# Kernel optimization log

Hardware: AMD Instinct MI355X
Metric: run time of the kernel (lower is better)

The kernel has to match this reference:

```python
import jax, jax.numpy as jnp
import numpy as np
from jax import lax

N = 20000; E = 640000
D_IN = 64; F1 = 256; H = 256
HEADS = 8; HC = 128; DH = HC // HEADS
NA = 8; MS = 64


def setup_inputs() -> dict:
    key = jax.random.key(0)
    ks = jax.random.split(key, 40)
    def w(k, shape, fan):
        return (jax.random.normal(k, shape, jnp.float32) / np.sqrt(fan)).astype(jnp.float32)
    inp = {}
    inp['state'] = jax.random.normal(ks[0], (N, D_IN), jnp.float32)
    inp['message'] = jax.random.normal(ks[1], (N, MS), jnp.float32)
    inp['edge_index'] = jax.random.randint(ks[2], (2, E), 0, N)
    # fc1 / fc2
    inp['W_fc1'] = w(ks[3], (D_IN, F1), D_IN); inp['b_fc1'] = jnp.zeros((F1,), jnp.float32)
    inp['W_fc2'] = w(ks[4], (MS, F1), MS);    inp['b_fc2'] = jnp.zeros((F1,), jnp.float32)
    # GRU: 2 layers, torch layout W_ih [3H, in], W_hh [3H, H]
    inp['Wih0'] = w(ks[5], (3 * H, F1), F1); inp['Whh0'] = w(ks[6], (3 * H, H), H)
    inp['bih0'] = jnp.zeros((3 * H,), jnp.float32); inp['bhh0'] = jnp.zeros((3 * H,), jnp.float32)
    inp['Wih1'] = w(ks[7], (3 * H, H), H); inp['Whh1'] = w(ks[8], (3 * H, H), H)
    inp['bih1'] = jnp.zeros((3 * H,), jnp.float32); inp['bhh1'] = jnp.zeros((3 * H,), jnp.float32)
    # GAT layer 1: in H -> HEADS heads of DH (concat -> HC)
    inp['Wg1'] = w(ks[9], (H, HC), H)
    inp['as1'] = w(ks[10], (HEADS, DH), DH); inp['ad1'] = w(ks[11], (HEADS, DH), DH)
    inp['bg1'] = jnp.zeros((HC,), jnp.float32)
    # GAT layer 2: HC -> HC
    inp['Wg2'] = w(ks[12], (HC, HC), HC)
    inp['as2'] = w(ks[13], (HEADS, DH), DH); inp['ad2'] = w(ks[14], (HEADS, DH), DH)
    inp['bg2'] = jnp.zeros((HC,), jnp.float32)
    # heads
    inp['Wc'] = w(ks[15], (HC, 1), HC); inp['bc'] = jnp.zeros((1,), jnp.float32)
    inp['Wmu'] = w(ks[16], (HC + H, NA), HC + H); inp['bmu'] = jnp.zeros((NA,), jnp.float32)
    inp['Wm'] = w(ks[17], (HC, MS), HC); inp['bm'] = jnp.zeros((MS,), jnp.float32)
    return inp


def gru_layer(x_seq, Wih, Whh, bih, bhh):
    # x_seq: [N, in]; torch GRUCell math, batch size 1 squeezed
    h_dim = Whh.shape[1]
    def step(h, x):
        gi = x @ Wih.T + bih
        gh = h @ Whh.T + bhh
        ir, iz, inn = jnp.split(gi, 3)
        hr, hz, hn = jnp.split(gh, 3)
        r = jax.nn.sigmoid(ir + hr)
        z = jax.nn.sigmoid(iz + hz)
        n = jnp.tanh(inn + r * hn)
        h_new = (1.0 - z) * n + z * h
        return h_new, h_new
    h0 = jnp.zeros((h_dim,), x_seq.dtype)
    _, ys = lax.scan(step, h0, x_seq)
    return ys  # [N, h_dim]


def gat_conv(x, W, a_src, a_dst, b, src, dst):
    # x: [N, in] -> [N, HEADS*DH], edge softmax over incoming edges per dst node
    n = x.shape[0]
    h = (x @ W).reshape(n, HEADS, DH)
    e_src = jnp.einsum('nhd,hd->nh', h, a_src)  # [N, HEADS]
    e_dst = jnp.einsum('nhd,hd->nh', h, a_dst)
    e = jax.nn.leaky_relu(e_src[src] + e_dst[dst], 0.2)  # [E, HEADS]
    emax = jax.ops.segment_max(e, dst, num_segments=n)
    emax = lax.stop_gradient(jnp.where(jnp.isfinite(emax), emax, 0.0))
    p = jnp.exp(e - emax[dst])
    denom = jax.ops.segment_sum(p, dst, num_segments=n)
    alpha = p / (denom[dst] + 1e-16)  # [E, HEADS]
    msgs = h[src] * alpha[:, :, None]  # [E, HEADS, DH]
    out = jax.ops.segment_sum(msgs, dst, num_segments=n)
    return out.reshape(n, HEADS * DH) + b


def reference(state, message, edge_index, W_fc1, b_fc1, W_fc2, b_fc2,
              Wih0, Whh0, bih0, bhh0, Wih1, Whh1, bih1, bhh1,
              Wg1, as1, ad1, bg1, Wg2, as2, ad2, bg2,
              Wc, bc, Wmu, bmu, Wm, bm):
    src, dst = edge_index[0], edge_index[1]
    x = jax.nn.relu(state @ W_fc1 + b_fc1)          # [N, F1]
    m = jax.nn.relu(message @ W_fc2 + b_fc2)        # [N, F1]
    x = x + m
    x = gru_layer(x, Wih0, Whh0, bih0, bhh0)        # [N, H]
    x = gru_layer(x, Wih1, Whh1, bih1, bhh1)
    x = jax.nn.relu(x)
    xg = gat_conv(x, Wg1, as1, ad1, bg1, src, dst)  # [N, HC]
    xg = jax.nn.relu(xg)
    xg = gat_conv(xg, Wg2, as2, ad2, bg2, src, dst)
    comm = jax.nn.sigmoid(xg @ Wc + bc)             # [N, 1]
    mu = jnp.tanh(jnp.concatenate([x, xg], axis=-1) @ Wmu + bmu)  # [N, NA]
    msg_out = jnp.tanh(xg @ Wm + bm)                # [N, MS]
    return comm, msg_out, mu
```

## Files before the change

### kernel.cpp

```cpp
#include <hip/hip_runtime.h>
#include <stdint.h>

#define N_NODES 20000
#define E_EDGES 640000
#define F1 256
#define HDIM 256
#define G3 768
#define HEADS 8
#define HC 128
#define DH 16
#define NA 8
#define MS 64

typedef _Float16 h2 __attribute__((ext_vector_type(2)));

__device__ __forceinline__ float fdot2(uint32_t a, uint32_t b, float c) {
#if __has_builtin(__builtin_amdgcn_fdot2)
  return __builtin_amdgcn_fdot2(__builtin_bit_cast(h2, a), __builtin_bit_cast(h2, b), c, false);
#else
  h2 x = __builtin_bit_cast(h2, a), y = __builtin_bit_cast(h2, b);
  return c + (float)x[0] * (float)y[0] + (float)x[1] * (float)y[1];
#endif
}

__device__ __forceinline__ float fexp2(float x) { return __builtin_amdgcn_exp2f(x); }
__device__ __forceinline__ float frcp(float x)  { return __builtin_amdgcn_rcpf(x); }
__device__ __forceinline__ float sigm(float x)  { return frcp(1.f + fexp2(-1.44269504f * x)); }
__device__ __forceinline__ float tanh_(float x) {
  x = fminf(20.f, fmaxf(-20.f, x));
  float t = fexp2(2.88539008f * x);
  return (t - 1.f) * frcp(t + 1.f);
}
__device__ __forceinline__ float leaky(float x) { return (x > 0.f) ? x : 0.2f * x; }
__device__ __forceinline__ unsigned fenc(float f) {
  unsigned u = __float_as_uint(f);
  return (u & 0x80000000u) ? ~u : (u | 0x80000000u);
}
__device__ __forceinline__ float fdec(unsigned u) {
  return __uint_as_float((u & 0x80000000u) ? (u ^ 0x80000000u) : ~u);
}

#define GF_BIAS 1
#define GF_RELU_OUT 2
#define GF_ACC 4
#define GF_RELU_A 8
#define GF_BT 16

template <int FLAGS>
__global__ __launch_bounds__(256) void gemm_k(const float* __restrict__ A,
                                              const float* __restrict__ B,
                                              const float* __restrict__ bias,
                                              float* __restrict__ C,
                                              int M, int K, int P) {
  __shared__ float As[64][68];
  __shared__ float Bs[64][68];
  int colTiles = P >> 6;
  int bx = blockIdx.x % colTiles;
  int by = blockIdx.x / colTiles;
  int row0 = by * 64, col0 = bx * 64;
  int tid = threadIdx.x;
  int tx = tid & 15, ty = tid >> 4;
  float acc[4][4] = {};
  for (int k0 = 0; k0 < K; k0 += 64) {
    {
      int r = tid >> 2, kq = (tid & 3) * 16;
      int gr = row0 + r;
      const float* ap = A + (size_t)gr * K + k0 + kq;
#pragma unroll
      for (int j = 0; j < 4; j++) {
        float4 v = make_float4(0.f, 0.f, 0.f, 0.f);
        if (gr < M) v = *(const float4*)(ap + 4 * j);
        if (FLAGS & GF_RELU_A) {
          v.x = fmaxf(v.x, 0.f); v.y = fmaxf(v.y, 0.f);
          v.z = fmaxf(v.z, 0.f); v.w = fmaxf(v.w, 0.f);
        }
        As[kq + 4 * j + 0][r] = v.x; As[kq + 4 * j + 1][r] = v.y;
        As[kq + 4 * j + 2][r] = v.z; As[kq + 4 * j + 3][r] = v.w;
      }
    }
    if (FLAGS & GF_BT) {
      int n = tid >> 2, kq = (tid & 3) * 16;
      const float* bp = B + (size_t)(col0 + n) * K + k0 + kq;
#pragma unroll
      for (int j = 0; j < 4; j++) {
        float4 v = *(const float4*)(bp + 4 * j);
        Bs[kq + 4 * j + 0][n] = v.x; Bs[kq + 4 * j + 1][n] = v.y;
        Bs[kq + 4 * j + 2][n] = v.z; Bs[kq + 4 * j + 3][n] = v.w;
      }
    } else {
      int kk = tid >> 2, nq = (tid & 3) * 16;
      const float* bp = B + (size_t)(k0 + kk) * P + col0 + nq;
#pragma unroll
      for (int j = 0; j < 4; j++)
        *(float4*)&Bs[kk][nq + 4 * j] = *(const float4*)(bp + 4 * j);
    }
    __syncthreads();
#pragma unroll
    for (int kk = 0; kk < 64; kk++) {
      float4 av = *(const float4*)&As[kk][ty * 4];
      float4 bv = *(const float4*)&Bs[kk][tx * 4];
      float a4[4] = {av.x, av.y, av.z, av.w};
      float b4[4] = {bv.x, bv.y, bv.z, bv.w};
#pragma unroll
      for (int i = 0; i < 4; i++)
#pragma unroll
        for (int j = 0; j < 4; j++) acc[i][j] = fmaf(a4[i], b4[j], acc[i][j]);
    }
    __syncthreads();
  }
#pragma unroll
  for (int i = 0; i < 4; i++) {
    int gr = row0 + ty * 4 + i;
    if (gr >= M) continue;
#pragma unroll
    for (int j = 0; j < 4; j++) {
      int gc = col0 + tx * 4 + j;
      float v = acc[i][j];
      if (FLAGS & GF_BIAS) v += bias[gc];
      if (FLAGS & GF_RELU_OUT) v = fmaxf(v, 0.f);
      size_t o = (size_t)gr * P + gc;
      if (FLAGS & GF_ACC) C[o] += v; else C[o] = v;
    }
  }
}

__global__ __launch_bounds__(256) void prep_w(const float* __restrict__ Whh,
                                              uint32_t* __restrict__ Wpk) {
  int idx = blockIdx.x * 256 + threadIdx.x;
  if (idx >= 48 * 2048) return;
  int i = idx >> 11;
  int rem = idx & 2047;
  int t = rem >> 2, comp = rem & 3;
  int q = 4 * i + comp;
  int g = t >> 2, c = t & 3;
  int a = q >> 5, p = q & 31;
  int row = (a % 3) * 256 + 2 * g + (a / 3);
  int k = 64 * c + 2 * p;
  h2 v = { (_Float16)Whh[row * 256 + k], (_Float16)Whh[row * 256 + k + 1] };
  Wpk[idx] = __builtin_bit_cast(uint32_t, v);
}

#define WD(i) uint4 W##i = Wp4[(i) * 512 + tid];
#define DOT6(A,B,C,D,E,F, m, hv) \
  a0 = fdot2(A.m, hv, a0); a1 = fdot2(B.m, hv, a1); a2 = fdot2(C.m, hv, a2); \
  a3 = fdot2(D.m, hv, a3); a4 = fdot2(E.m, hv, a4); a5 = fdot2(F.m, hv, a5);
#define DOT4(H, A,B,C,D,E,F) \
  DOT6(A,B,C,D,E,F, x, H.x) DOT6(A,B,C,D,E,F, y, H.y) \
  DOT6(A,B,C,D,E,F, z, H.z) DOT6(A,B,C,D,E,F, w, H.w)

__global__ __launch_bounds__(512, 2) void gru_scan(const float* __restrict__ GI,
                                                   const uint32_t* __restrict__ Wpk,
                                                   const float* __restrict__ bhh,
                                                   float* __restrict__ Hout) {
  __shared__ __align__(16) uint32_t hb[2][4][36];
  int tid = threadIdx.x;
  int g = tid >> 2, c = tid & 3;
  int lane = tid & 63;
  const uint4* Wp4 = (const uint4*)Wpk;
  WD(0)  WD(1)  WD(2)  WD(3)  WD(4)  WD(5)  WD(6)  WD(7)
  WD(8)  WD(9)  WD(10) WD(11) WD(12) WD(13) WD(14) WD(15)
  WD(16) WD(17) WD(18) WD(19) WD(20) WD(21) WD(22) WD(23)
  WD(24) WD(25) WD(26) WD(27) WD(28) WD(29) WD(30) WD(31)
  WD(32) WD(33) WD(34) WD(35) WD(36) WD(37) WD(38) WD(39)
  WD(40) WD(41) WD(42) WD(43) WD(44) WD(45) WD(46) WD(47)
  for (int i = tid; i < 2 * 4 * 36; i += 512) ((uint32_t*)hb)[i] = 0;
  bool gatel = ((c & 1) == 0);
  int j = 2 * g + (c >> 1);
  float bh_r = 0, bh_z = 0, bh_n = 0, hreg = 0, gr = 0, gz = 0, gn = 0;
  if (gatel) {
    bh_r = bhh[j]; bh_z = bhh[256 + j]; bh_n = bhh[512 + j];
    gr = GI[j]; gz = GI[256 + j]; gn = GI[512 + j];
  }
  __syncthreads();
  int buf = 0;
  const int bl = lane & ~3;
#pragma unroll 1
  for (int t = 0; t < N_NODES; t++) {
    float pgr = 0, pgz = 0, pgn = 0;
    if (gatel) {
      int tn = (t + 1 < N_NODES) ? t + 1 : t;
      const float* gp = GI + (size_t)tn * G3;
      pgr = gp[j]; pgz = gp[256 + j]; pgn = gp[512 + j];
    }
    float a0 = 0, a1 = 0, a2 = 0, a3 = 0, a4 = 0, a5 = 0;
    const uint4* hc4 = (const uint4*)(&hb[buf][c][0]);
    uint4 Ha = hc4[0];
    uint4 Hb = hc4[1];
    DOT4(Ha, W0, W8,  W16, W24, W32, W40)  Ha = hc4[2];
    DOT4(Hb, W1, W9,  W17, W25, W33, W41)  Hb = hc4[3];
    DOT4(Ha, W2, W10, W18, W26, W34, W42)  Ha = hc4[4];
    DOT4(Hb, W3, W11, W19, W27, W35, W43)  Hb = hc4[5];
    DOT4(Ha, W4, W12, W20, W28, W36, W44)  Ha = hc4[6];
    DOT4(Hb, W5, W13, W21, W29, W37, W45)  Hb = hc4[7];
    DOT4(Ha, W6, W14, W22, W30, W38, W46)
    DOT4(Hb, W7, W15, W23, W31, W39, W47)
    float v6 = 0.f, v7 = 0.f;
    float u0, u1, u2, u3;
    {
      float t0 = __shfl_xor(a0, 2, 64), t4 = __shfl_xor(a4, 2, 64);
      u0 = (c & 2) ? a4 + t4 : a0 + t0;
      float t1 = __shfl_xor(a1, 2, 64), t5 = __shfl_xor(a5, 2, 64);
      u1 = (c & 2) ? a5 + t5 : a1 + t1;
      float t2 = __shfl_xor(a2, 2, 64), t6 = __shfl_xor(v6, 2, 64);
      u2 = (c & 2) ? v6 + t6 : a2 + t2;
      float t3 = __shfl_xor(a3, 2, 64), t7 = __shfl_xor(v7, 2, 64);
      u3 = (c & 2) ? v7 + t7 : a3 + t3;
    }
    float f0, f1;
    {
      float t0 = __shfl_xor(u0, 1, 64), t2 = __shfl_xor(u2, 1, 64);
      f0 = (c & 1) ? u2 + t2 : u0 + t0;
      float t1 = __shfl_xor(u1, 1, 64), t3 = __shfl_xor(u3, 1, 64);
      f1 = (c & 1) ? u3 + t3 : u1 + t1;
    }
    float ta = __shfl(f0, bl + 1, 64);
    float tb = __shfl(f1, bl + 1, 64);
    if (gatel) {
      float Sr = (c == 0) ? f0 : tb;
      float Sz = (c == 0) ? f1 : f0;
      float Sn = (c == 0) ? ta : f1;
      float r = sigm(gr + bh_r + Sr);
      float z = sigm(gz + bh_z + Sz);
      float n = tanh_(gn + r * (Sn + bh_n));
      float hn = (1.f - z) * n + z * hreg;
      hreg = hn;
      Hout[(size_t)t * HDIM + j] = hn;
      int pj = j >> 1, cc = pj >> 5, half = j & 1;
      ushort* hw = (ushort*)&hb[buf ^ 1][cc][0];
      hw[(pj & 31) * 2 + half] = __builtin_bit_cast(uint16_t, (_Float16)hn);
      gr = pgr; gz = pgz; gn = pgn;
    }
    __syncthreads();
    buf ^= 1;
  }
}

__global__ __launch_bounds__(256) void esed_k(const float* __restrict__ Hg,
                                              const float* __restrict__ a_s,
                                              const float* __restrict__ a_d,
                                              float* __restrict__ es, float* __restrict__ ed) {
  int idx = blockIdx.x * 256 + threadIdx.x;
  if (idx >= N_NODES * HEADS) return;
  int n = idx >> 3, hd = idx & 7;
  const float* hp = Hg + (size_t)n * HC + hd * DH;
  float s = 0, d = 0;
#pragma unroll
  for (int i = 0; i < DH; i++) {
    float h = hp[i];
    s = fmaf(h, a_s[hd * DH + i], s);
    d = fmaf(h, a_d[hd * DH + i], d);
  }
  es[idx] = s; ed[idx] = d;
}

__global__ __launch_bounds__(256) void esmax_k(const float* __restrict__ es,
                                               unsigned* __restrict__ m) {
  int idx = blockIdx.x * 256 + threadIdx.x;
  float v = (idx < N_NODES * HEADS) ? es[idx] : -1e30f;
#pragma unroll
  for (int mask = 32; mask >= 8; mask >>= 1) v = fmaxf(v, __shfl_xor(v, mask, 64));
  if ((threadIdx.x & 63) < 8) atomicMax(&m[threadIdx.x & 7], fenc(v));
}

__global__ __launch_bounds__(256) void deg_k(const int* __restrict__ ei, int* __restrict__ deg) {
  int e = blockIdx.x * 256 + threadIdx.x;
  if (e >= E_EDGES) return;
  atomicAdd(&deg[ei[E_EDGES + e]], 1);
}

__global__ __launch_bounds__(1024) void scan_k(const int* __restrict__ deg, int* __restrict__ off) {
  __shared__ int wsum[16];
  __shared__ int carry;
  int tid = threadIdx.x, lane = tid & 63, wv = tid >> 6;
  if (tid == 0) carry = 0;
  __syncthreads();
  for (int base = 0; base < N_NODES; base += 1024) {
    int i = base + tid;
    int v = (i < N_NODES) ? deg[i] : 0;
    int s = v;
#pragma unroll
    for (int d = 1; d < 64; d <<= 1) {
      int t = __shfl_up(s, d, 64);
      if (lane >= d) s += t;
    }
    if (lane == 63) wsum[wv] = s;
    __syncthreads();
    if (wv == 0 && lane < 16) {
      int t = wsum[lane];
#pragma unroll
      for (int d = 1; d < 16; d <<= 1) {
        int u = __shfl_up(t, d, 64);
        if (lane >= d) t += u;
      }
      wsum[lane] = t;
    }
    __syncthreads();
    int prev = (wv > 0) ? wsum[wv - 1] : 0;
    int excl = carry + prev + s - v;
    if (i < N_NODES) off[i] = excl;
    int total = wsum[15];
    __syncthreads();
    if (tid == 0) carry += total;
    __syncthreads();
  }
  if (tid == 0) off[N_NODES] = carry;
}

__global__ __launch_bounds__(256) void scatter_k(const int* __restrict__ ei,
                                                 const int* __restrict__ off,
                                                 int* __restrict__ cnt,
                                                 int* __restrict__ csr_src) {
  int e = blockIdx.x * 256 + threadIdx.x;
  if (e >= E_EDGES) return;
  int d = ei[E_EDGES + e];
  int pos = off[d] + atomicAdd(&cnt[d], 1);
  csr_src[pos] = ei[e];
}

template <int RELU>
__global__ __launch_bounds__(256) void gather_k(const int* __restrict__ off,
                                                const int* __restrict__ csr_src,
                                                const float* __restrict__ es,
                                                const float* __restrict__ ed,
                                                const unsigned* __restrict__ esm,
                                                const float* __restrict__ Hg,
                                                const float* __restrict__ bias,
                                                float* __restrict__ out) {
  int wv = threadIdx.x >> 6, lane = threadIdx.x & 63;
  int d = blockIdx.x * 4 + wv;
  if (d >= N_NODES) return;
  int hd0 = lane >> 4, hd1 = 4 + (lane >> 4);
  float ed0 = ed[d * 8 + hd0], ed1 = ed[d * 8 + hd1];
  float cb0 = leaky(fdec(esm[hd0]) + ed0);
  float cb1 = leaky(fdec(esm[hd1]) + ed1);
  int e0 = off[d], e1 = off[d + 1];
  float acc0 = 0, acc1 = 0, den0 = 0, den1 = 0;
  for (int i = e0; i < e1; i++) {
    int s = csr_src[i];
    float p0 = fexp2(1.44269504f * (leaky(es[s * 8 + hd0] + ed0) - cb0));
    float p1 = fexp2(1.44269504f * (leaky(es[s * 8 + hd1] + ed1) - cb1));
    float h0 = Hg[(size_t)s * HC + lane];
    float h1 = Hg[(size_t)s * HC + 64 + lane];
    acc0 = fmaf(p0, h0, acc0); acc1 = fmaf(p1, h1, acc1);
    den0 += p0; den1 += p1;
  }
  float o0 = acc0 * frcp(den0 + 1e-16f);
  float o1 = acc1 * frcp(den1 + 1e-16f);
  if (RELU) {
    o0 = fmaxf(o0 + bias[lane], 0.f);
    o1 = fmaxf(o1 + bias[64 + lane], 0.f);
  }
  out[(size_t)d * HC + lane] = o0;
  out[(size_t)d * HC + 64 + lane] = o1;
}

__global__ __launch_bounds__(64) void heads_k(const float* __restrict__ xgb,
                                              const float* __restrict__ bg2,
                                              const float* __restrict__ H2,
                                              const float* __restrict__ Wc, const float* __restrict__ bc,
                                              const float* __restrict__ Wmu, const float* __restrict__ bmu,
                                              const float* __restrict__ Wm, const float* __restrict__ bm,
                                              float* __restrict__ out) {
  int n = blockIdx.x, l = threadIdx.x;
  __shared__ float xg[HC];
  __shared__ float xr[HDIM];
  for (int i = l; i < HC; i += 64) xg[i] = xgb[(size_t)n * HC + i] + bg2[i];
  for (int i = l; i < HDIM; i += 64) xr[i] = fmaxf(H2[(size_t)n * HDIM + i], 0.f);
  __syncthreads();
  float acc = bm[l];
#pragma unroll 8
  for (int k = 0; k < HC; k++) acc = fmaf(xg[k], Wm[k * MS + l], acc);
  out[N_NODES + (size_t)n * MS + l] = tanh_(acc);
  if (l < NA) {
    float a = bmu[l];
    for (int k = 0; k < HDIM; k++) a = fmaf(xr[k], Wmu[k * NA + l], a);
    for (int k = 0; k < HC; k++) a = fmaf(xg[k], Wmu[(HDIM + k) * NA + l], a);
    out[N_NODES + (size_t)N_NODES * MS + (size_t)n * NA + l] = tanh_(a);
  }
  if (l == 0) {
    float a = bc[0];
    for (int k = 0; k < HC; k++) a = fmaf(xg[k], Wc[k], a);
    out[n] = sigm(a);
  }
}

extern "C" void kernel_launch(void* const* d_in, const int* in_sizes, int n_in,
                              void* d_out, int out_size, void* d_ws, size_t ws_size,
                              hipStream_t stream) {
  const float* state = (const float*)d_in[0];
  const float* message = (const float*)d_in[1];
  const int* ei = (const int*)d_in[2];
  const float* Wfc1 = (const float*)d_in[3]; const float* bfc1 = (const float*)d_in[4];
  const float* Wfc2 = (const float*)d_in[5]; const float* bfc2 = (const float*)d_in[6];
  const float* Wih0 = (const float*)d_in[7]; const float* Whh0 = (const float*)d_in[8];
  const float* bih0 = (const float*)d_in[9]; const float* bhh0 = (const float*)d_in[10];
  const float* Wih1 = (const float*)d_in[11]; const float* Whh1 = (const float*)d_in[12];
  const float* bih1 = (const float*)d_in[13]; const float* bhh1 = (const float*)d_in[14];
  const float* Wg1 = (const float*)d_in[15]; const float* as1 = (const float*)d_in[16];
  const float* ad1 = (const float*)d_in[17]; const float* bg1 = (const float*)d_in[18];
  const float* Wg2 = (const float*)d_in[19]; const float* as2 = (const float*)d_in[20];
  const float* ad2 = (const float*)d_in[21]; const float* bg2 = (const float*)d_in[22];
  const float* Wc = (const float*)d_in[23]; const float* bc = (const float*)d_in[24];
  const float* Wmu = (const float*)d_in[25]; const float* bmu = (const float*)d_in[26];
  const float* Wm = (const float*)d_in[27]; const float* bm = (const float*)d_in[28];

  float* ws = (float*)d_ws;
  float* GI = ws;
  float* HGa = ws;
  float* HGb = ws + 2560000;
  float* X2  = ws + 5120000;
  float* ES  = ws + 7680000;
  float* ED  = ws + 7840000;
  unsigned* ESM = (unsigned*)(ws + 8160000);
  int* DEG = (int*)(ws + 8200000);
  int* OFF = (int*)(ws + 8230000);
  int* CNT = (int*)(ws + 8260000);
  int* CSR = (int*)(ws + 8300000);
  float* X  = ws + 15360000;
  float* H2 = ws + 20480000;
  uint32_t* Wpk = (uint32_t*)(ws + 25600000);
  float* out = (float*)d_out;

  int rt = (N_NODES + 63) / 64;

  gemm_k<GF_BIAS | GF_RELU_OUT><<<rt * 4, 256, 0, stream>>>(state, Wfc1, bfc1, X, N_NODES, 64, 256);
  gemm_k<GF_BIAS | GF_RELU_OUT | GF_ACC><<<rt * 4, 256, 0, stream>>>(message, Wfc2, bfc2, X, N_NODES, 64, 256);
  gemm_k<GF_BIAS | GF_BT><<<rt * 12, 256, 0, stream>>>(X, Wih0, bih0, GI, N_NODES, 256, G3);
  prep_w<<<384, 256, 0, stream>>>(Whh0, Wpk);
  gru_scan<<<1, 512, 0, stream>>>(GI, Wpk, bhh0, X);
  gemm_k<GF_BIAS | GF_BT><<<rt * 12, 256, 0, stream>>>(X, Wih1, bih1, GI, N_NODES, 256, G3);
  prep_w<<<384, 256, 0, stream>>>(Whh1, Wpk);
  gru_scan<<<1, 512, 0, stream>>>(GI, Wpk, bhh1, H2);
  hipMemsetAsync(DEG, 0, N_NODES * 4, stream);
  hipMemsetAsync(CNT, 0, N_NODES * 4, stream);
  deg_k<<<2500, 256, 0, stream>>>(ei, DEG);
  scan_k<<<1, 1024, 0, stream>>>(DEG, OFF);
  scatter_k<<<2500, 256, 0, stream>>>(ei, OFF, CNT, CSR);
  gemm_k<GF_RELU_A><<<rt * 2, 256, 0, stream>>>(H2, Wg1, nullptr, HGa, N_NODES, 256, HC);
  esed_k<<<625, 256, 0, stream>>>(HGa, as1, ad1, ES, ED);
  hipMemsetAsync(ESM, 0, 8 * 4, stream);
  esmax_k<<<625, 256, 0, stream>>>(ES, ESM);
  gather_k<1><<<5000, 256, 0, stream>>>(OFF, CSR, ES, ED, ESM, HGa, bg1, X2);
  gemm_k<0><<<rt * 2, 256, 0, stream>>>(X2, Wg2, nullptr, HGa, N_NODES, HC, HC);
  esed_k<<<625, 256, 0, stream>>>(HGa, as2, ad2, ES, ED);
  hipMemsetAsync(ESM, 0, 8 * 4, stream);
  esmax_k<<<625, 256, 0, stream>>>(ES, ESM);
  gather_k<0><<<5000, 256, 0, stream>>>(OFF, CSR, ES, ED, ESM, HGa, nullptr, HGb);
  heads_k<<<N_NODES, 64, 0, stream>>>(HGb, bg2, H2, Wc, bc, Wmu, bmu, Wm, bm, out);
}
```

Baseline: 58.39 ms.

## Pin GRU recurrent weights to fixed VGPRs via inline asm dot2

Rewrites the GRU scan inner loop so the packed fp16 recurrent weights sit in hard-coded VGPRs v64-v255 and are consumed by inline-asm v_dot2_f32_f16. This keeps the compiler from spilling or shuffling them. The r/z hidden biases are folded into the input-gate GEMM bias by a new prep_b kernel, and the next-step GI prefetch is dropped. The scan now launches 64 redundant blocks with only block 0 writing output, apparently to raise clocks or occupancy, at the cost of extra power and L2 traffic. Hard-coded register names combined with asm clobbers are fragile.

```diff
diff --git a/kernel.cpp b/kernel.cpp
--- a/kernel.cpp
+++ b/kernel.cpp
@@ -13,15 +13,6 @@
 #define MS 64
 
 typedef _Float16 h2 __attribute__((ext_vector_type(2)));
-
-__device__ __forceinline__ float fdot2(uint32_t a, uint32_t b, float c) {
-#if __has_builtin(__builtin_amdgcn_fdot2)
-  return __builtin_amdgcn_fdot2(__builtin_bit_cast(h2, a), __builtin_bit_cast(h2, b), c, false);
-#else
-  h2 x = __builtin_bit_cast(h2, a), y = __builtin_bit_cast(h2, b);
-  return c + (float)x[0] * (float)y[0] + (float)x[1] * (float)y[1];
-#endif
-}
 
 __device__ __forceinline__ float fexp2(float x) { return __builtin_amdgcn_exp2f(x); }
 __device__ __forceinline__ float frcp(float x)  { return __builtin_amdgcn_rcpf(x); }
@@ -140,60 +131,118 @@
   Wpk[idx] = __builtin_bit_cast(uint32_t, v);
 }
 
-#define WD(i) uint4 W##i = Wp4[(i) * 512 + tid];
-#define DOT6(A,B,C,D,E,F, m, hv) \
-  a0 = fdot2(A.m, hv, a0); a1 = fdot2(B.m, hv, a1); a2 = fdot2(C.m, hv, a2); \
-  a3 = fdot2(D.m, hv, a3); a4 = fdot2(E.m, hv, a4); a5 = fdot2(F.m, hv, a5);
-#define DOT4(H, A,B,C,D,E,F) \
-  DOT6(A,B,C,D,E,F, x, H.x) DOT6(A,B,C,D,E,F, y, H.y) \
-  DOT6(A,B,C,D,E,F, z, H.z) DOT6(A,B,C,D,E,F, w, H.w)
-
-__global__ __launch_bounds__(512, 2) void gru_scan(const float* __restrict__ GI,
-                                                   const uint32_t* __restrict__ Wpk,
-                                                   const float* __restrict__ bhh,
-                                                   float* __restrict__ Hout) {
+__global__ __launch_bounds__(256) void prep_b(const float* __restrict__ bih,
+                                              const float* __restrict__ bhh,
+                                              float* __restrict__ b2) {
+  int i = blockIdx.x * 256 + threadIdx.x;
+  if (i < G3) b2[i] = bih[i] + (i < 512 ? bhh[i] : 0.f);
+}
+
+#define WLOAD(i, R0, R1, R2, R3) do { uint4 w_ = Wp4[(i) * 512 + tid]; \
+  asm volatile("v_mov_b32 " R0 ", %0\n\tv_mov_b32 " R1 ", %1\n\tv_mov_b32 " R2 \
+               ", %2\n\tv_mov_b32 " R3 ", %3" \
+               :: "v"(w_.x), "v"(w_.y), "v"(w_.z), "v"(w_.w) : R0, R1, R2, R3); } while (0)
+
+#define DOTM(HX, A0, A1, A2, A3, A4, A5) \
+  asm volatile("v_dot2_f32_f16 %0, " A0 ", %6, %0\n\t" \
+               "v_dot2_f32_f16 %1, " A1 ", %6, %1\n\t" \
+               "v_dot2_f32_f16 %2, " A2 ", %6, %2\n\t" \
+               "v_dot2_f32_f16 %3, " A3 ", %6, %3\n\t" \
+               "v_dot2_f32_f16 %4, " A4 ", %6, %4\n\t" \
+               "v_dot2_f32_f16 %5, " A5 ", %6, %5" \
+               : "+v"(a0), "+v"(a1), "+v"(a2), "+v"(a3), "+v"(a4), "+v"(a5) \
+               : "v"(HX));
+
+__global__ __launch_bounds__(512) void gru_scan(const float* __restrict__ GI,
+                                                const uint32_t* __restrict__ Wpk,
+                                                const float* __restrict__ bhh,
+                                                float* __restrict__ Hout) {
   __shared__ __align__(16) uint32_t hb[2][4][36];
   int tid = threadIdx.x;
   int g = tid >> 2, c = tid & 3;
   int lane = tid & 63;
   const uint4* Wp4 = (const uint4*)Wpk;
-  WD(0)  WD(1)  WD(2)  WD(3)  WD(4)  WD(5)  WD(6)  WD(7)
-  WD(8)  WD(9)  WD(10) WD(11) WD(12) WD(13) WD(14) WD(15)
-  WD(16) WD(17) WD(18) WD(19) WD(20) WD(21) WD(22) WD(23)
-  WD(24) WD(25) WD(26) WD(27) WD(28) WD(29) WD(30) WD(31)
-  WD(32) WD(33) WD(34) WD(35) WD(36) WD(37) WD(38) WD(39)
-  WD(40) WD(41) WD(42) WD(43) WD(44) WD(45) WD(46) WD(47)
+  WLOAD(0,"v64","v65","v66","v67");     WLOAD(1,"v68","v69","v70","v71");
+  WLOAD(2,"v72","v73","v74","v75");     WLOAD(3,"v76","v77","v78","v79");
+  WLOAD(4,"v80","v81","v82","v83");     WLOAD(5,"v84","v85","v86","v87");
+  WLOAD(6,"v88","v89","v90","v91");     WLOAD(7,"v92","v93","v94","v95");
+  WLOAD(8,"v96","v97","v98","v99");     WLOAD(9,"v100","v101","v102","v103");
+  WLOAD(10,"v104","v105","v106","v107"); WLOAD(11,"v108","v109","v110","v111");
+  WLOAD(12,"v112","v113","v114","v115"); WLOAD(13,"v116","v117","v118","v119");
+  WLOAD(14,"v120","v121","v122","v123"); WLOAD(15,"v124","v125","v126","v127");
+  WLOAD(16,"v128","v129","v130","v131"); WLOAD(17,"v132","v133","v134","v135");
+  WLOAD(18,"v136","v137","v138","v139"); WLOAD(19,"v140","v141","v142","v143");
+  WLOAD(20,"v144","v145","v146","v147"); WLOAD(21,"v148","v149","v150","v151");
+  WLOAD(22,"v152","v153","v154","v155"); WLOAD(23,"v156","v157","v158","v159");
+  WLOAD(24,"v160","v161","v162","v163"); WLOAD(25,"v164","v165","v166","v167");
+  WLOAD(26,"v168","v169","v170","v171"); WLOAD(27,"v172","v173","v174","v175");
+  WLOAD(28,"v176","v177","v178","v179"); WLOAD(29,"v180","v181","v182","v183");
+  WLOAD(30,"v184","v185","v186","v187"); WLOAD(31,"v188","v189","v190","v191");
+  WLOAD(32,"v192","v193","v194","v195"); WLOAD(33,"v196","v197","v198","v199");
+  WLOAD(34,"v200","v201","v202","v203"); WLOAD(35,"v204","v205","v206","v207");
+  WLOAD(36,"v208","v209","v210","v211"); WLOAD(37,"v212","v213","v214","v215");
+  WLOAD(38,"v216","v217","v218","v219"); WLOAD(39,"v220","v221","v222","v223");
+  WLOAD(40,"v224","v225","v226","v227"); WLOAD(41,"v228","v229","v230","v231");
+  WLOAD(42,"v232","v233","v234","v235"); WLOAD(43,"v236","v237","v238","v239");
+  WLOAD(44,"v240","v241","v242","v243"); WLOAD(45,"v244","v245","v246","v247");
+  WLOAD(46,"v248","v249","v250","v251"); WLOAD(47,"v252","v253","v254","v255");
   for (int i = tid; i < 2 * 4 * 36; i += 512) ((uint32_t*)hb)[i] = 0;
+  bool wr = (blockIdx.x == 0);
   bool gatel = ((c & 1) == 0);
   int j = 2 * g + (c >> 1);
-  float bh_r = 0, bh_z = 0, bh_n = 0, hreg = 0, gr = 0, gz = 0, gn = 0;
-  if (gatel) {
-    bh_r = bhh[j]; bh_z = bhh[256 + j]; bh_n = bhh[512 + j];
-    gr = GI[j]; gz = GI[256 + j]; gn = GI[512 + j];
-  }
+  float bh_n = 0.f, hreg = 0.f;
+  if (gatel) bh_n = bhh[512 + j];
   __syncthreads();
   int buf = 0;
   const int bl = lane & ~3;
 #pragma unroll 1
   for (int t = 0; t < N_NODES; t++) {
-    float pgr = 0, pgz = 0, pgn = 0;
+    float gr = 0.f, gz = 0.f, gn = 0.f;
     if (gatel) {
-      int tn = (t + 1 < N_NODES) ? t + 1 : t;
-      const float* gp = GI + (size_t)tn * G3;
-      pgr = gp[j]; pgz = gp[256 + j]; pgn = gp[512 + j];
-    }
-    float a0 = 0, a1 = 0, a2 = 0, a3 = 0, a4 = 0, a5 = 0;
+      const float* gp = GI + (size_t)t * G3;
+      gr = gp[j]; gz = gp[256 + j]; gn = gp[512 + j];
+    }
+    float a0 = 0.f, a1 = 0.f, a2 = 0.f, a3 = 0.f, a4 = 0.f, a5 = 0.f;
     const uint4* hc4 = (const uint4*)(&hb[buf][c][0]);
-    uint4 Ha = hc4[0];
-    uint4 Hb = hc4[1];
-    DOT4(Ha, W0, W8,  W16, W24, W32, W40)  Ha = hc4[2];
-    DOT4(Hb, W1, W9,  W17, W25, W33, W41)  Hb = hc4[3];
-    DOT4(Ha, W2, W10, W18, W26, W34, W42)  Ha = hc4[4];
-    DOT4(Hb, W3, W11, W19, W27, W35, W43)  Hb = hc4[5];
-    DOT4(Ha, W4, W12, W20, W28, W36, W44)  Ha = hc4[6];
-    DOT4(Hb, W5, W13, W21, W29, W37, W45)  Hb = hc4[7];
-    DOT4(Ha, W6, W14, W22, W30, W38, W46)
-    DOT4(Hb, W7, W15, W23, W31, W39, W47)
+    uint4 Ha = hc4[0], Hb = hc4[1];
+    DOTM(Ha.x,"v64","v96","v128","v160","v192","v224")
+    DOTM(Ha.y,"v65","v97","v129","v161","v193","v225")
+    DOTM(Ha.z,"v66","v98","v130","v162","v194","v226")
+    DOTM(Ha.w,"v67","v99","v131","v163","v195","v227")
+    Ha = hc4[2];
+    DOTM(Hb.x,"v68","v100","v132","v164","v196","v228")
+    DOTM(Hb.y,"v69","v101","v133","v165","v197","v229")
+    DOTM(Hb.z,"v70","v102","v134","v166","v198","v230")
+    DOTM(Hb.w,"v71","v103","v135","v167","v199","v231")
+    Hb = hc4[3];
+    DOTM(Ha.x,"v72","v104","v136","v168","v200","v232")
+    DOTM(Ha.y,"v73","v105","v137","v169","v201","v233")
+    DOTM(Ha.z,"v74","v106","v138","v170","v202","v234")
+    DOTM(Ha.w,"v75","v107","v139","v171","v203","v235")
+    Ha = hc4[4];
+    DOTM(Hb.x,"v76","v108","v140","v172","v204","v236")
+    DOTM(Hb.y,"v77","v109","v141","v173","v205","v237")
+    DOTM(Hb.z,"v78","v110","v142","v174","v206","v238")
+    DOTM(Hb.w,"v79","v111","v143","v175","v207","v239")
+    Hb = hc4[5];
+    DOTM(Ha.x,"v80","v112","v144","v176","v208","v240")
+    DOTM(Ha.y,"v81","v113","v145","v177","v209","v241")
+    DOTM(Ha.z,"v82","v114","v146","v178","v210","v242")
+    DOTM(Ha.w,"v83","v115","v147","v179","v211","v243")
+    Ha = hc4[6];
+    DOTM(Hb.x,"v84","v116","v148","v180","v212","v244")
+    DOTM(Hb.y,"v85","v117","v149","v181","v213","v245")
+    DOTM(Hb.z,"v86","v118","v150","v182","v214","v246")
+    DOTM(Hb.w,"v87","v119","v151","v183","v215","v247")
+    Hb = hc4[7];
+    DOTM(Ha.x,"v88","v120","v152","v184","v216","v248")
+    DOTM(Ha.y,"v89","v121","v153","v185","v217","v249")
+    DOTM(Ha.z,"v90","v122","v154","v186","v218","v250")
+    DOTM(Ha.w,"v91","v123","v155","v187","v219","v251")
+    DOTM(Hb.x,"v92","v124","v156","v188","v220","v252")
+    DOTM(Hb.y,"v93","v125","v157","v189","v221","v253")
+    DOTM(Hb.z,"v94","v126","v158","v190","v222","v254")
+    DOTM(Hb.w,"v95","v127","v159","v191","v223","v255")
     float v6 = 0.f, v7 = 0.f;
     float u0, u1, u2, u3;
     {
@@ -219,16 +268,15 @@
       float Sr = (c == 0) ? f0 : tb;
       float Sz = (c == 0) ? f1 : f0;
       float Sn = (c == 0) ? ta : f1;
-      float r = sigm(gr + bh_r + Sr);
-      float z = sigm(gz + bh_z + Sz);
+      float r = sigm(gr + Sr);
+      float z = sigm(gz + Sz);
       float n = tanh_(gn + r * (Sn + bh_n));
       float hn = (1.f - z) * n + z * hreg;
       hreg = hn;
-      Hout[(size_t)t * HDIM + j] = hn;
+      if (wr) Hout[(size_t)t * HDIM + j] = hn;
       int pj = j >> 1, cc = pj >> 5, half = j & 1;
       ushort* hw = (ushort*)&hb[buf ^ 1][cc][0];
       hw[(pj & 31) * 2 + half] = __builtin_bit_cast(uint16_t, (_Float16)hn);
-      gr = pgr; gz = pgz; gn = pgn;
     }
     __syncthreads();
     buf ^= 1;
@@ -418,6 +466,7 @@
   int* CSR = (int*)(ws + 8300000);
   float* X  = ws + 15360000;
   float* H2 = ws + 20480000;
+  float* B2  = H2;
   uint32_t* Wpk = (uint32_t*)(ws + 25600000);
   float* out = (float*)d_out;
 
@@ -425,12 +474,14 @@
 
   gemm_k<GF_BIAS | GF_RELU_OUT><<<rt * 4, 256, 0, stream>>>(state, Wfc1, bfc1, X, N_NODES, 64, 256);
   gemm_k<GF_BIAS | GF_RELU_OUT | GF_ACC><<<rt * 4, 256, 0, stream>>>(message, Wfc2, bfc2, X, N_NODES, 64, 256);
-  gemm_k<GF_BIAS | GF_BT><<<rt * 12, 256, 0, stream>>>(X, Wih0, bih0, GI, N_NODES, 256, G3);
+  prep_b<<<3, 256, 0, stream>>>(bih0, bhh0, B2);
+  gemm_k<GF_BIAS | GF_BT><<<rt * 12, 256, 0, stream>>>(X, Wih0, B2, GI, N_NODES, 256, G3);
   prep_w<<<384, 256, 0, stream>>>(Whh0, Wpk);
-  gru_scan<<<1, 512, 0, stream>>>(GI, Wpk, bhh0, X);
-  gemm_k<GF_BIAS | GF_BT><<<rt * 12, 256, 0, stream>>>(X, Wih1, bih1, GI, N_NODES, 256, G3);
+  gru_scan<<<64, 512, 0, stream>>>(GI, Wpk, bhh0, X);
+  prep_b<<<3, 256, 0, stream>>>(bih1, bhh1, B2);
+  gemm_k<GF_BIAS | GF_BT><<<rt * 12, 256, 0, stream>>>(X, Wih1, B2, GI, N_NODES, 256, G3);
   prep_w<<<384, 256, 0, stream>>>(Whh1, Wpk);
-  gru_scan<<<1, 512, 0, stream>>>(GI, Wpk, bhh1, H2);
+  gru_scan<<<64, 512, 0, stream>>>(GI, Wpk, bhh1, H2);
   hipMemsetAsync(DEG, 0, N_NODES * 4, stream);
   hipMemsetAsync(CNT, 0, N_NODES * 4, stream);
   deg_k<<<2500, 256, 0, stream>>>(ei, DEG);
```

Measured after the change: 60.87 ms. +4.2%, slower.
